# Kernel tuning notes

Measured on AMD Instinct MI355X. Metric: run time of the kernel, lower is better.

The kernel has to match this reference:

```python
import jax, jax.numpy as jnp
import numpy as np

E = 8   # num_experts
K = 2   # top-k


def setup_inputs() -> dict:
    key = jax.random.key(0)
    ks = jax.random.split(key, 5)
    T, D, H = 8192, 512, 1024
    s = lambda n: 1.0 / np.sqrt(n)
    return {
        "x": jax.random.normal(ks[0], (T, D), jnp.float32),
        "Wg": jax.random.normal(ks[1], (D, E), jnp.float32) * s(D),   # gating weights (no bias)
        "W1": jax.random.normal(ks[2], (E, D, H), jnp.float32) * s(D),  # expert first layer
        "b1": jnp.zeros((E, H), jnp.float32),
        "W2": jax.random.normal(ks[3], (E, H, D), jnp.float32) * s(H),  # expert output layer
        "b2": jnp.zeros((E, D), jnp.float32),
    }


def reference(x, Wg, W1, b1, W2, b2):
    T = x.shape[0]
    eps = 1e-10
    # --- noisy gating (eval mode: no noise) ---
    logits = x @ Wg                                   # [T, E]
    # top_k THEN softmax (apply_softmax_before_top_k=False default)
    top_vals, top_idx = jax.lax.top_k(logits, K)      # [T, K]
    top_probs = jax.nn.softmax(top_vals, axis=-1)
    rows = jnp.arange(T)[:, None]
    gate_probs = jnp.zeros((T, E), x.dtype).at[rows, top_idx].add(top_probs)  # scatter_add
    khot = jnp.zeros((T, E), x.dtype).at[rows, top_idx].set(1.0)
    # --- expert MLPs (dense equivalent of dispatch/compute/combine:
    #     tokens not routed to an expert get weight 0, identical math) ---
    h = jax.nn.relu(jnp.einsum('td,edh->teh', x, W1) + b1)  # [T, E, H]
    eo = jnp.einsum('teh,ehd->ted', h, W2) + b2             # [T, E, D]
    out = jnp.einsum('ted,te->td', eo, gate_probs)          # weighted combine
    # --- load-balancing losses (torch .var() is unbiased -> ddof=1) ---
    importance = gate_probs.sum(axis=0)
    importance_loss = jnp.var(importance, ddof=1) / (importance.mean() ** 2 + eps)
    load = khot.sum(axis=0)  # eval-mode load = token counts per expert
    load_loss = jnp.var(load, ddof=1) / (load.mean() ** 2 + eps)
    return out, importance_loss, load_loss
```

## Files before the change

### kernel.cpp

```cpp
#include <hip/hip_runtime.h>
#include <math.h>

#define T_TOK 8192
#define D_DIM 512
#define H_DIM 1024
#define NE    8
#define NHB   64

typedef __attribute__((ext_vector_type(8))) short bf16x8;
typedef __attribute__((ext_vector_type(4))) float f32x4;
typedef __attribute__((ext_vector_type(4))) unsigned short us4;
typedef __attribute__((ext_vector_type(8))) unsigned short us8;


__device__ __forceinline__ unsigned short f2bf(float f) {
  union { float f; unsigned int u; } v; v.f = f;
  const unsigned int u = v.u;
  return (unsigned short)((u + 0x7fffu + ((u >> 16) & 1u)) >> 16);
}

__device__ __forceinline__ float bf2f(unsigned short b) {
  union { unsigned int u; float f; } v; v.u = ((unsigned int)b) << 16;
  return v.f;
}

__device__ __forceinline__ void gload16(const void* g, void* l) {
  __builtin_amdgcn_global_load_lds(
      (const __attribute__((address_space(1))) void*)g,
      (__attribute__((address_space(3))) void*)l, 16, 0, 0);
}

__global__ __launch_bounds__(256) void cvt_x_kernel(const float* __restrict__ x,
                                                    unsigned short* __restrict__ xb) {
  const int i = (blockIdx.x * 256 + threadIdx.x) * 8;
  const float4 a = *reinterpret_cast<const float4*>(&x[i]);
  const float4 b = *reinterpret_cast<const float4*>(&x[i + 4]);
  us8 o;
  o[0] = f2bf(a.x); o[1] = f2bf(a.y); o[2] = f2bf(a.z); o[3] = f2bf(a.w);
  o[4] = f2bf(b.x); o[5] = f2bf(b.y); o[6] = f2bf(b.z); o[7] = f2bf(b.w);
  *reinterpret_cast<us8*>(&xb[i]) = o;
}

__global__ __launch_bounds__(256) void wtrans_kernel(
    const float* __restrict__ W1, const float* __restrict__ W2,
    unsigned short* __restrict__ W1T, unsigned short* __restrict__ W2T) {
  __shared__ unsigned short lds[32][36];
  int bid = blockIdx.x;
  const float* src; unsigned short* dst; int R, C, lc;
  if (bid < 4096) { src = W1; dst = W1T; R = D_DIM; C = H_DIM; lc = 5; }
  else { bid -= 4096; src = W2; dst = W2T; R = H_DIM; C = D_DIM; lc = 4; }
  const int e = bid >> 9;
  const int rem = bid & 511;
  const int rt = rem >> lc;
  const int ct = rem & ((C >> 5) - 1);
  const size_t ebase = (size_t)e * R * C;
  const int tid = threadIdx.x;
  {
    const int r = tid >> 3, c0 = (tid & 7) * 4;
    const float4 v = *reinterpret_cast<const float4*>(
        &src[ebase + (size_t)(rt * 32 + r) * C + ct * 32 + c0]);
    lds[r][c0 + 0] = f2bf(v.x); lds[r][c0 + 1] = f2bf(v.y);
    lds[r][c0 + 2] = f2bf(v.z); lds[r][c0 + 3] = f2bf(v.w);
  }
  __syncthreads();
  {
    const int c = tid >> 3, r0 = (tid & 7) * 4;
    us4 o;
    o[0] = lds[r0 + 0][c]; o[1] = lds[r0 + 1][c];
    o[2] = lds[r0 + 2][c]; o[3] = lds[r0 + 3][c];
    *reinterpret_cast<us4*>(&dst[ebase + (size_t)(ct * 32 + c) * R + rt * 32 + r0]) = o;
  }
}

__global__ __launch_bounds__(256) void gating_kernel(
    const float* __restrict__ x, const float* __restrict__ Wg,
    int* __restrict__ top_e, float* __restrict__ top_p)
{
  __shared__ float wgs[NE][D_DIM];
  const int tid = threadIdx.x;
  for (int i = tid; i < D_DIM * NE; i += 256)
    wgs[i & 7][i >> 3] = Wg[i];
  __syncthreads();

  const int lane = tid & 63;
  const int wave = tid >> 6;
  const int t = blockIdx.x * 4 + wave;

  float acc[NE];
#pragma unroll
  for (int e = 0; e < NE; e++) acc[e] = 0.f;
#pragma unroll
  for (int j = 0; j < 8; j++) {
    const int d = lane + j * 64;
    const float xv = x[(size_t)t * D_DIM + d];
#pragma unroll
    for (int e = 0; e < NE; e++) acc[e] += xv * wgs[e][d];
  }
#pragma unroll
  for (int e = 0; e < NE; e++) {
#pragma unroll
    for (int m = 32; m > 0; m >>= 1) acc[e] += __shfl_xor(acc[e], m);
  }

  if (lane == 0) {
    int i0 = 0; float v0 = acc[0];
#pragma unroll
    for (int e = 1; e < NE; e++) if (acc[e] > v0) { v0 = acc[e]; i0 = e; }
    int i1 = -1; float v1 = -3.4e38f;
#pragma unroll
    for (int e = 0; e < NE; e++) if (e != i0 && acc[e] > v1) { v1 = acc[e]; i1 = e; }

    const float ex = __expf(v1 - v0);
    const float inv = 1.f / (1.f + ex);
    top_e[t * 2 + 0] = i0; top_e[t * 2 + 1] = i1;
    top_p[t * 2 + 0] = inv; top_p[t * 2 + 1] = ex * inv;
  }
}

__global__ __launch_bounds__(256) void hist_kernel(
    const int* __restrict__ top_e, const float* __restrict__ top_p,
    int* __restrict__ hist, float* __restrict__ impp)
{
  __shared__ int   h[NE];
  __shared__ float im[NE];
  const int tid = threadIdx.x;
  if (tid < NE) { h[tid] = 0; im[tid] = 0.f; }
  __syncthreads();
  const int i = blockIdx.x * 256 + tid;
  const int e = top_e[i];
  atomicAdd(&h[e], 1);
  atomicAdd(&im[e], top_p[i]);
  __syncthreads();
  if (tid < NE) {
    hist[blockIdx.x * NE + tid] = h[tid];
    impp[blockIdx.x * NE + tid] = im[tid];
  }
}

__global__ void finalize_kernel(const int* __restrict__ hist,
                                const float* __restrict__ impp,
                                int* __restrict__ counts, float* __restrict__ importance,
                                int* __restrict__ offsets, int* __restrict__ bb,
                                float* __restrict__ out_tail)
{
  __shared__ int   cnt_s[NE];
  __shared__ float imp_s[NE];
  __shared__ int   off_s[NE];
  const int tid = threadIdx.x;
  if (tid < NE) {
    int c = 0; float s = 0.f;
    for (int b = 0; b < NHB; b++) { c += hist[b * NE + tid]; s += impp[b * NE + tid]; }
    cnt_s[tid] = c; imp_s[tid] = s;
    counts[tid] = c; importance[tid] = s;
  }
  __syncthreads();
  if (tid == 0) {
    int off = 0;
    for (int e = 0; e < NE; e++) { off_s[e] = off; offsets[e] = off; off += cnt_s[e]; }
    float mi = 0.f, ml = 0.f;
    for (int e = 0; e < NE; e++) { mi += imp_s[e]; ml += (float)cnt_s[e]; }
    mi *= (1.f / NE); ml *= (1.f / NE);
    float vi = 0.f, vl = 0.f;
    for (int e = 0; e < NE; e++) {
      const float di = imp_s[e] - mi; vi += di * di;
      const float dl = (float)cnt_s[e] - ml; vl += dl * dl;
    }
    vi *= (1.f / (NE - 1)); vl *= (1.f / (NE - 1));
    out_tail[0] = vi / (mi * mi + 1e-10f);
    out_tail[1] = vl / (ml * ml + 1e-10f);
  }
  __syncthreads();
  if (tid < NE) {
    int run = off_s[tid];
    for (int b = 0; b < NHB; b++) { bb[b * NE + tid] = run; run += hist[b * NE + tid]; }
  }
}

__global__ __launch_bounds__(256) void scatter_kernel(
    const int* __restrict__ top_e, const float* __restrict__ top_p,
    const int* __restrict__ bb,
    int* __restrict__ tok_list, int* __restrict__ inv_slot)
{
  __shared__ int cur[NE];
  const int tid = threadIdx.x;
  if (tid < NE) cur[tid] = bb[blockIdx.x * NE + tid];
  __syncthreads();
  const int i = blockIdx.x * 256 + tid;
  const int e = top_e[i];
  const int pos = atomicAdd(&cur[e], 1);
  tok_list[pos] = i >> 1;
  inv_slot[i] = pos;
}

template<int KD, int MTILES, bool STAGE2>
__global__ __launch_bounds__(256) void expert_gemm_kernel(
    const unsigned short* __restrict__ Wt,
    const unsigned short* __restrict__ Bsrc,
    const float* __restrict__ bias,
    const int* __restrict__ counts, const int* __restrict__ offsets,
    const int* __restrict__ tok_list,
    unsigned short* __restrict__ Hout)
{
  constexpr int M = MTILES * 128;
  constexpr int LMT = (MTILES == 8) ? 3 : 2;
  constexpr int OD = STAGE2 ? D_DIM : H_DIM;
  const int e = blockIdx.x & 7;
  const int tmp = blockIdx.x >> 3;
  const int mtile = tmp & (MTILES - 1);
  const int ttile = tmp >> LMT;
  const int cnt = counts[e];
  if (ttile * 128 >= cnt) return;
  const int base = offsets[e] + ttile * 128;
  const int rem = cnt - ttile * 128;
  const int nvalid = rem < 128 ? rem : 128;

  __shared__ unsigned short Ws[128][64];
  __shared__ unsigned short Xs[128][64];

  const int tid = threadIdx.x;
  const int lane = tid & 63;
  const int wave = tid >> 6;
  const int wm = wave & 1, wn = wave >> 1;

  const unsigned short* wsrc[4];
  const unsigned short* bsrc[4];
#pragma unroll
  for (int i = 0; i < 4; i++) {
    const int seg = tid + i * 256;
    const int row = seg >> 3;
    const int s = seg & 7;
    const int scol = ((s ^ (row & 7)) << 3);
    wsrc[i] = Wt + ((size_t)e * M + (size_t)(mtile * 128 + row)) * KD + scol;
    const int cr = (row < nvalid) ? row : (nvalid - 1);
    const int brow = STAGE2 ? (base + cr) : tok_list[base + cr];
    bsrc[i] = Bsrc + (size_t)brow * KD + scol;
  }
  unsigned short* ws0 = &Ws[0][0];
  unsigned short* xs0 = &Xs[0][0];
  const int ldso = wave * 512;

  f32x4 acc[4][4];
#pragma unroll
  for (int mi = 0; mi < 4; mi++)
#pragma unroll
    for (int nj = 0; nj < 4; nj++)
#pragma unroll
      for (int q = 0; q < 4; q++) acc[mi][nj][q] = 0.f;

  for (int k0 = 0; k0 < KD; k0 += 64) {
#pragma unroll
    for (int i = 0; i < 4; i++) {
      gload16(wsrc[i] + k0, ws0 + ldso + i * 2048);
      gload16(bsrc[i] + k0, xs0 + ldso + i * 2048);
    }
    __syncthreads();
#pragma unroll
    for (int ks = 0; ks < 2; ks++) {
      bf16x8 a[4], b[4];
#pragma unroll
      for (int mi = 0; mi < 4; mi++) {
        const int m = wm * 64 + mi * 16 + (lane & 15);
        const int sl = ((ks * 4 + (lane >> 4)) ^ (m & 7)) << 3;
        a[mi] = *reinterpret_cast<const bf16x8*>(&Ws[m][sl]);
      }
#pragma unroll
      for (int nj = 0; nj < 4; nj++) {
        const int r = wn * 64 + nj * 16 + (lane & 15);
        const int sl = ((ks * 4 + (lane >> 4)) ^ (r & 7)) << 3;
        b[nj] = *reinterpret_cast<const bf16x8*>(&Xs[r][sl]);
      }
#pragma unroll
      for (int mi = 0; mi < 4; mi++)
#pragma unroll
        for (int nj = 0; nj < 4; nj++)
          acc[mi][nj] = __builtin_amdgcn_mfma_f32_16x16x32_bf16(a[mi], b[nj], acc[mi][nj], 0, 0, 0);
    }
    __syncthreads();
  }

#pragma unroll
  for (int mi = 0; mi < 4; mi++) {
    const int mb = mtile * 128 + wm * 64 + mi * 16 + ((lane >> 4) << 2);
    float bv[4];
#pragma unroll
    for (int j = 0; j < 4; j++) bv[j] = bias[e * M + mb + j];
#pragma unroll
    for (int nj = 0; nj < 4; nj++) {
      const int r = wn * 64 + nj * 16 + (lane & 15);
      if (r < nvalid) {
        us4 o;
#pragma unroll
        for (int j = 0; j < 4; j++) {
          const float v = acc[mi][nj][j] + bv[j];
          o[j] = f2bf(STAGE2 ? v : fmaxf(v, 0.f));
        }
        *reinterpret_cast<us4*>(&Hout[(size_t)(base + r) * OD + mb]) = o;
      }
    }
  }
}

__global__ __launch_bounds__(256) void combine_kernel(
    const unsigned short* __restrict__ EO,
    const int* __restrict__ inv_slot, const float* __restrict__ top_p,
    float* __restrict__ out)
{
  const int idx = blockIdx.x * 256 + threadIdx.x;
  const int t  = idx >> 6;
  const int d0 = (idx & 63) * 8;
  const int s0 = inv_slot[t * 2 + 0];
  const int s1 = inv_slot[t * 2 + 1];
  const float p0 = top_p[t * 2 + 0];
  const float p1 = top_p[t * 2 + 1];
  const us8 a = *reinterpret_cast<const us8*>(&EO[(size_t)s0 * D_DIM + d0]);
  const us8 b = *reinterpret_cast<const us8*>(&EO[(size_t)s1 * D_DIM + d0]);
  float4 o0, o1;
  o0.x = p0 * bf2f(a[0]) + p1 * bf2f(b[0]);
  o0.y = p0 * bf2f(a[1]) + p1 * bf2f(b[1]);
  o0.z = p0 * bf2f(a[2]) + p1 * bf2f(b[2]);
  o0.w = p0 * bf2f(a[3]) + p1 * bf2f(b[3]);
  o1.x = p0 * bf2f(a[4]) + p1 * bf2f(b[4]);
  o1.y = p0 * bf2f(a[5]) + p1 * bf2f(b[5]);
  o1.z = p0 * bf2f(a[6]) + p1 * bf2f(b[6]);
  o1.w = p0 * bf2f(a[7]) + p1 * bf2f(b[7]);
  float* op = &out[(size_t)t * D_DIM + d0];
  *reinterpret_cast<float4*>(op)     = o0;
  *reinterpret_cast<float4*>(op + 4) = o1;
}

extern "C" void kernel_launch(void* const* d_in, const int* in_sizes, int n_in,
                              void* d_out, int out_size, void* d_ws, size_t ws_size,
                              hipStream_t stream)
{
  const float* x  = (const float*)d_in[0];
  const float* Wg = (const float*)d_in[1];
  const float* W1 = (const float*)d_in[2];
  const float* b1 = (const float*)d_in[3];
  const float* W2 = (const float*)d_in[4];
  const float* b2 = (const float*)d_in[5];
  float* out = (float*)d_out;

  char* ws = (char*)d_ws;
  int*   counts     = (int*)(ws + 0);
  float* importance = (float*)(ws + 32);
  int*   offsets    = (int*)(ws + 64);
  int*   top_e      = (int*)(ws + 128);
  float* top_p      = (float*)(ws + 128 + 65536);
  int*   tok_list   = (int*)(ws + 128 + 131072);
  int*   hist       = (int*)(ws + 262400);
  float* impp       = (float*)(ws + 264448);
  int*   bb         = (int*)(ws + 266496);
  int*   inv_slot   = (int*)(ws + 268544);
  unsigned short* XB   = (unsigned short*)(ws + (1ull << 20));
  unsigned short* W1T  = (unsigned short*)(ws + (9ull << 20));
  unsigned short* W2T  = (unsigned short*)(ws + (17ull << 20));
  unsigned short* HBUF = (unsigned short*)(ws + (25ull << 20));
  unsigned short* EO   = (unsigned short*)(ws + (1ull << 20));

  cvt_x_kernel<<<2048, 256, 0, stream>>>(x, XB);
  wtrans_kernel<<<8192, 256, 0, stream>>>(W1, W2, W1T, W2T);
  gating_kernel<<<T_TOK / 4, 256, 0, stream>>>(x, Wg, top_e, top_p);
  hist_kernel<<<NHB, 256, 0, stream>>>(top_e, top_p, hist, impp);
  finalize_kernel<<<1, 64, 0, stream>>>(hist, impp, counts, importance, offsets, bb,
                                        out + (size_t)T_TOK * D_DIM);
  scatter_kernel<<<NHB, 256, 0, stream>>>(top_e, top_p, bb, tok_list, inv_slot);
  expert_gemm_kernel<512, 8, false><<<8 * 8 * 64, 256, 0, stream>>>(
      W1T, XB, b1, counts, offsets, tok_list, HBUF);
  expert_gemm_kernel<1024, 4, true><<<8 * 4 * 64, 256, 0, stream>>>(
      W2T, HBUF, b2, counts, offsets, tok_list, EO);
  combine_kernel<<<T_TOK * D_DIM / (256 * 8), 256, 0, stream>>>(EO, inv_slot, top_p, out);
}
```

Baseline: 208.4 us.

## Fuse x conversion and histogram into gating, double-buffer expert GEMM, widen transpose tiles

```diff
diff --git a/kernel.cpp b/kernel.cpp
--- a/kernel.cpp
+++ b/kernel.cpp
@@ -5,7 +5,8 @@
 #define D_DIM 512
 #define H_DIM 1024
 #define NE    8
-#define NHB   64
+#define NGB   2048
+#define NSB   64
 
 typedef __attribute__((ext_vector_type(8))) short bf16x8;
 typedef __attribute__((ext_vector_type(4))) float f32x4;
@@ -30,110 +31,98 @@
       (__attribute__((address_space(3))) void*)l, 16, 0, 0);
 }
 
-__global__ __launch_bounds__(256) void cvt_x_kernel(const float* __restrict__ x,
-                                                    unsigned short* __restrict__ xb) {
-  const int i = (blockIdx.x * 256 + threadIdx.x) * 8;
-  const float4 a = *reinterpret_cast<const float4*>(&x[i]);
-  const float4 b = *reinterpret_cast<const float4*>(&x[i + 4]);
-  us8 o;
-  o[0] = f2bf(a.x); o[1] = f2bf(a.y); o[2] = f2bf(a.z); o[3] = f2bf(a.w);
-  o[4] = f2bf(b.x); o[5] = f2bf(b.y); o[6] = f2bf(b.z); o[7] = f2bf(b.w);
-  *reinterpret_cast<us8*>(&xb[i]) = o;
+__global__ __launch_bounds__(256) void gating_kernel(
+    const float* __restrict__ x, const float* __restrict__ Wg,
+    unsigned short* __restrict__ XB,
+    int* __restrict__ top_e, float* __restrict__ top_p,
+    int* __restrict__ hist, float* __restrict__ impp)
+{
+  __shared__ float wgs[NE][D_DIM];
+  __shared__ int   h[NE];
+  __shared__ float im[NE];
+  const int tid = threadIdx.x;
+  for (int i = tid; i < D_DIM * NE; i += 256)
+    wgs[i & 7][i >> 3] = Wg[i];
+  if (tid < NE) { h[tid] = 0; im[tid] = 0.f; }
+  __syncthreads();
+
+  const int lane = tid & 63;
+  const int wave = tid >> 6;
+  const int t = blockIdx.x * 4 + wave;
+
+  float acc[NE];
+#pragma unroll
+  for (int e = 0; e < NE; e++) acc[e] = 0.f;
+#pragma unroll
+  for (int j = 0; j < 8; j++) {
+    const int d = lane + j * 64;
+    const float xv = x[(size_t)t * D_DIM + d];
+    XB[(size_t)t * D_DIM + d] = f2bf(xv);
+#pragma unroll
+    for (int e = 0; e < NE; e++) acc[e] += xv * wgs[e][d];
+  }
+#pragma unroll
+  for (int e = 0; e < NE; e++) {
+#pragma unroll
+    for (int m = 32; m > 0; m >>= 1) acc[e] += __shfl_xor(acc[e], m);
+  }
+
+  if (lane == 0) {
+    int i0 = 0; float v0 = acc[0];
+#pragma unroll
+    for (int e = 1; e < NE; e++) if (acc[e] > v0) { v0 = acc[e]; i0 = e; }
+    int i1 = -1; float v1 = -3.4e38f;
+#pragma unroll
+    for (int e = 0; e < NE; e++) if (e != i0 && acc[e] > v1) { v1 = acc[e]; i1 = e; }
+
+    const float ex = __expf(v1 - v0);
+    const float inv = 1.f / (1.f + ex);
+    const float p0 = inv, p1 = ex * inv;
+    top_e[t * 2 + 0] = i0; top_e[t * 2 + 1] = i1;
+    top_p[t * 2 + 0] = p0; top_p[t * 2 + 1] = p1;
+    atomicAdd(&h[i0], 1);  atomicAdd(&h[i1], 1);
+    atomicAdd(&im[i0], p0); atomicAdd(&im[i1], p1);
+  }
+  __syncthreads();
+  if (tid < NE) {
+    hist[blockIdx.x * NE + tid] = h[tid];
+    impp[blockIdx.x * NE + tid] = im[tid];
+  }
 }
 
 __global__ __launch_bounds__(256) void wtrans_kernel(
     const float* __restrict__ W1, const float* __restrict__ W2,
     unsigned short* __restrict__ W1T, unsigned short* __restrict__ W2T) {
-  __shared__ unsigned short lds[32][36];
+  __shared__ unsigned short lds[64][76];
   int bid = blockIdx.x;
   const float* src; unsigned short* dst; int R, C, lc;
-  if (bid < 4096) { src = W1; dst = W1T; R = D_DIM; C = H_DIM; lc = 5; }
-  else { bid -= 4096; src = W2; dst = W2T; R = H_DIM; C = D_DIM; lc = 4; }
-  const int e = bid >> 9;
-  const int rem = bid & 511;
+  if (bid < 1024) { src = W1; dst = W1T; R = D_DIM; C = H_DIM; lc = 4; }
+  else { bid -= 1024; src = W2; dst = W2T; R = H_DIM; C = D_DIM; lc = 3; }
+  const int e = bid >> 7;
+  const int rem = bid & 127;
   const int rt = rem >> lc;
-  const int ct = rem & ((C >> 5) - 1);
+  const int ct = rem & ((C >> 6) - 1);
   const size_t ebase = (size_t)e * R * C;
   const int tid = threadIdx.x;
-  {
-    const int r = tid >> 3, c0 = (tid & 7) * 4;
+#pragma unroll
+  for (int it = 0; it < 4; it++) {
+    const int idx = it * 256 + tid;
+    const int r = idx >> 4, c0 = (idx & 15) * 4;
     const float4 v = *reinterpret_cast<const float4*>(
-        &src[ebase + (size_t)(rt * 32 + r) * C + ct * 32 + c0]);
-    lds[r][c0 + 0] = f2bf(v.x); lds[r][c0 + 1] = f2bf(v.y);
-    lds[r][c0 + 2] = f2bf(v.z); lds[r][c0 + 3] = f2bf(v.w);
-  }
-  __syncthreads();
-  {
-    const int c = tid >> 3, r0 = (tid & 7) * 4;
-    us4 o;
-    o[0] = lds[r0 + 0][c]; o[1] = lds[r0 + 1][c];
-    o[2] = lds[r0 + 2][c]; o[3] = lds[r0 + 3][c];
-    *reinterpret_cast<us4*>(&dst[ebase + (size_t)(ct * 32 + c) * R + rt * 32 + r0]) = o;
-  }
-}
-
-__global__ __launch_bounds__(256) void gating_kernel(
-    const float* __restrict__ x, const float* __restrict__ Wg,
-    int* __restrict__ top_e, float* __restrict__ top_p)
-{
-  __shared__ float wgs[NE][D_DIM];
-  const int tid = threadIdx.x;
-  for (int i = tid; i < D_DIM * NE; i += 256)
-    wgs[i & 7][i >> 3] = Wg[i];
-  __syncthreads();
-
-  const int lane = tid & 63;
-  const int wave = tid >> 6;
-  const int t = blockIdx.x * 4 + wave;
-
-  float acc[NE];
-#pragma unroll
-  for (int e = 0; e < NE; e++) acc[e] = 0.f;
-#pragma unroll
-  for (int j = 0; j < 8; j++) {
-    const int d = lane + j * 64;
-    const float xv = x[(size_t)t * D_DIM + d];
-#pragma unroll
-    for (int e = 0; e < NE; e++) acc[e] += xv * wgs[e][d];
-  }
-#pragma unroll
-  for (int e = 0; e < NE; e++) {
-#pragma unroll
-    for (int m = 32; m > 0; m >>= 1) acc[e] += __shfl_xor(acc[e], m);
-  }
-
-  if (lane == 0) {
-    int i0 = 0; float v0 = acc[0];
-#pragma unroll
-    for (int e = 1; e < NE; e++) if (acc[e] > v0) { v0 = acc[e]; i0 = e; }
-    int i1 = -1; float v1 = -3.4e38f;
-#pragma unroll
-    for (int e = 0; e < NE; e++) if (e != i0 && acc[e] > v1) { v1 = acc[e]; i1 = e; }
-
-    const float ex = __expf(v1 - v0);
-    const float inv = 1.f / (1.f + ex);
-    top_e[t * 2 + 0] = i0; top_e[t * 2 + 1] = i1;
-    top_p[t * 2 + 0] = inv; top_p[t * 2 + 1] = ex * inv;
-  }
-}
-
-__global__ __launch_bounds__(256) void hist_kernel(
-    const int* __restrict__ top_e, const float* __restrict__ top_p,
-    int* __restrict__ hist, float* __restrict__ impp)
-{
-  __shared__ int   h[NE];
-  __shared__ float im[NE];
-  const int tid = threadIdx.x;
-  if (tid < NE) { h[tid] = 0; im[tid] = 0.f; }
-  __syncthreads();
-  const int i = blockIdx.x * 256 + tid;
-  const int e = top_e[i];
-  atomicAdd(&h[e], 1);
-  atomicAdd(&im[e], top_p[i]);
-  __syncthreads();
-  if (tid < NE) {
-    hist[blockIdx.x * NE + tid] = h[tid];
-    impp[blockIdx.x * NE + tid] = im[tid];
+        &src[ebase + (size_t)(rt * 64 + r) * C + ct * 64 + c0]);
+    us4 o; o[0] = f2bf(v.x); o[1] = f2bf(v.y); o[2] = f2bf(v.z); o[3] = f2bf(v.w);
+    *reinterpret_cast<us4*>(&lds[r][c0]) = o;
+  }
+  __syncthreads();
+#pragma unroll
+  for (int it = 0; it < 2; it++) {
+    const int idx = it * 256 + tid;
+    const int dc = idx >> 3;
+    const int c8 = idx & 7;
+    us8 o;
+#pragma unroll
+    for (int m = 0; m < 8; m++) o[m] = lds[c8 * 8 + m][dc];
+    *reinterpret_cast<us8*>(&dst[ebase + (size_t)(ct * 64 + dc) * R + rt * 64 + c8 * 8]) = o;
   }
 }
 
@@ -149,7 +138,7 @@
   const int tid = threadIdx.x;
   if (tid < NE) {
     int c = 0; float s = 0.f;
-    for (int b = 0; b < NHB; b++) { c += hist[b * NE + tid]; s += impp[b * NE + tid]; }
+    for (int b = 0; b < NGB; b++) { c += hist[b * NE + tid]; s += impp[b * NE + tid]; }
     cnt_s[tid] = c; imp_s[tid] = s;
     counts[tid] = c; importance[tid] = s;
   }
@@ -172,13 +161,15 @@
   __syncthreads();
   if (tid < NE) {
     int run = off_s[tid];
-    for (int b = 0; b < NHB; b++) { bb[b * NE + tid] = run; run += hist[b * NE + tid]; }
+    for (int g = 0; g < NGB; g++) {
+      if ((g & 31) == 0) bb[(g >> 5) * NE + tid] = run;
+      run += hist[g * NE + tid];
+    }
   }
 }
 
 __global__ __launch_bounds__(256) void scatter_kernel(
-    const int* __restrict__ top_e, const float* __restrict__ top_p,
-    const int* __restrict__ bb,
+    const int* __restrict__ top_e, const int* __restrict__ bb,
     int* __restrict__ tok_list, int* __restrict__ inv_slot)
 {
   __shared__ int cur[NE];
@@ -204,6 +195,7 @@
   constexpr int M = MTILES * 128;
   constexpr int LMT = (MTILES == 8) ? 3 : 2;
   constexpr int OD = STAGE2 ? D_DIM : H_DIM;
+  constexpr int NK = KD / 64;
   const int e = blockIdx.x & 7;
   const int tmp = blockIdx.x >> 3;
   const int mtile = tmp & (MTILES - 1);
@@ -214,8 +206,8 @@
   const int rem = cnt - ttile * 128;
   const int nvalid = rem < 128 ? rem : 128;
 
-  __shared__ unsigned short Ws[128][64];
-  __shared__ unsigned short Xs[128][64];
+  __shared__ unsigned short Ws[2][128][64];
+  __shared__ unsigned short Xs[2][128][64];
 
   const int tid = threadIdx.x;
   const int lane = tid & 63;
@@ -235,8 +227,6 @@
     const int brow = STAGE2 ? (base + cr) : tok_list[base + cr];
     bsrc[i] = Bsrc + (size_t)brow * KD + scol;
   }
-  unsigned short* ws0 = &Ws[0][0];
-  unsigned short* xs0 = &Xs[0][0];
   const int ldso = wave * 512;
 
   f32x4 acc[4][4];
@@ -247,13 +237,24 @@
 #pragma unroll
       for (int q = 0; q < 4; q++) acc[mi][nj][q] = 0.f;
 
-  for (int k0 = 0; k0 < KD; k0 += 64) {
-#pragma unroll
-    for (int i = 0; i < 4; i++) {
-      gload16(wsrc[i] + k0, ws0 + ldso + i * 2048);
-      gload16(bsrc[i] + k0, xs0 + ldso + i * 2048);
-    }
-    __syncthreads();
+#pragma unroll
+  for (int i = 0; i < 4; i++) {
+    gload16(wsrc[i], &Ws[0][0][0] + ldso + i * 2048);
+    gload16(bsrc[i], &Xs[0][0][0] + ldso + i * 2048);
+  }
+  __syncthreads();
+
+#pragma unroll 2
+  for (int it = 0; it < NK; ++it) {
+    const int cur = it & 1;
+    if (it + 1 < NK) {
+      const int k0 = (it + 1) * 64;
+#pragma unroll
+      for (int i = 0; i < 4; i++) {
+        gload16(wsrc[i] + k0, &Ws[cur ^ 1][0][0] + ldso + i * 2048);
+        gload16(bsrc[i] + k0, &Xs[cur ^ 1][0][0] + ldso + i * 2048);
+      }
+    }
 #pragma unroll
     for (int ks = 0; ks < 2; ks++) {
       bf16x8 a[4], b[4];
@@ -261,13 +262,13 @@
       for (int mi = 0; mi < 4; mi++) {
         const int m = wm * 64 + mi * 16 + (lane & 15);
         const int sl = ((ks * 4 + (lane >> 4)) ^ (m & 7)) << 3;
-        a[mi] = *reinterpret_cast<const bf16x8*>(&Ws[m][sl]);
+        a[mi] = *reinterpret_cast<const bf16x8*>(&Ws[cur][m][sl]);
       }
 #pragma unroll
       for (int nj = 0; nj < 4; nj++) {
         const int r = wn * 64 + nj * 16 + (lane & 15);
         const int sl = ((ks * 4 + (lane >> 4)) ^ (r & 7)) << 3;
-        b[nj] = *reinterpret_cast<const bf16x8*>(&Xs[r][sl]);
+        b[nj] = *reinterpret_cast<const bf16x8*>(&Xs[cur][r][sl]);
       }
 #pragma unroll
       for (int mi = 0; mi < 4; mi++)
@@ -348,25 +349,23 @@
   float* top_p      = (float*)(ws + 128 + 65536);
   int*   tok_list   = (int*)(ws + 128 + 131072);
   int*   hist       = (int*)(ws + 262400);
-  float* impp       = (float*)(ws + 264448);
-  int*   bb         = (int*)(ws + 266496);
-  int*   inv_slot   = (int*)(ws + 268544);
+  float* impp       = (float*)(ws + 328064);
+  int*   bb         = (int*)(ws + 393728);
+  int*   inv_slot   = (int*)(ws + 395776);
   unsigned short* XB   = (unsigned short*)(ws + (1ull << 20));
   unsigned short* W1T  = (unsigned short*)(ws + (9ull << 20));
   unsigned short* W2T  = (unsigned short*)(ws + (17ull << 20));
   unsigned short* HBUF = (unsigned short*)(ws + (25ull << 20));
   unsigned short* EO   = (unsigned short*)(ws + (1ull << 20));
 
-  cvt_x_kernel<<<2048, 256, 0, stream>>>(x, XB);
-  wtrans_kernel<<<8192, 256, 0, stream>>>(W1, W2, W1T, W2T);
-  gating_kernel<<<T_TOK / 4, 256, 0, stream>>>(x, Wg, top_e, top_p);
-  hist_kernel<<<NHB, 256, 0, stream>>>(top_e, top_p, hist, impp);
+  gating_kernel<<<NGB, 256, 0, stream>>>(x, Wg, XB, top_e, top_p, hist, impp);
+  wtrans_kernel<<<2048, 256, 0, stream>>>(W1, W2, W1T, W2T);
   finalize_kernel<<<1, 64, 0, stream>>>(hist, impp, counts, importance, offsets, bb,
                                         out + (size_t)T_TOK * D_DIM);
-  scatter_kernel<<<NHB, 256, 0, stream>>>(top_e, top_p, bb, tok_list, inv_slot);
-  expert_gemm_kernel<512, 8, false><<<8 * 8 * 64, 256, 0, stream>>>(
+  scatter_kernel<<<NSB, 256, 0, stream>>>(top_e, bb, tok_list, inv_slot);
+  expert_gemm_kernel<512, 8, false><<<8 * 8 * 128, 256, 0, stream>>>(
       W1T, XB, b1, counts, offsets, tok_list, HBUF);
-  expert_gemm_kernel<1024, 4, true><<<8 * 4 * 64, 256, 0, stream>>>(
+  expert_gemm_kernel<1024, 4, true><<<8 * 4 * 128, 256, 0, stream>>>(
       W2T, HBUF, b2, counts, offsets, tok_list, EO);
   combine_kernel<<<T_TOK * D_DIM / (256 * 8), 256, 0, stream>>>(EO, inv_slot, top_p, out);
 }
```

New measurement: 325.1 us. 1.56x slower.
